# Optimization experiments

Measured on AMD Instinct MI355X. Metric: run time of the kernel, lower is better.

The kernel has to match this reference:

```python
import jax, jax.numpy as jnp
import numpy as np

NUM_EXPERT = 16
IN_FEAT = 1024
OUT_FEAT = 1024
BATCH = 8192


def setup_inputs() -> dict:
    key = jax.random.key(0)
    k_inp, k_gate, k_w = jax.random.split(key, 3)
    inp = jax.random.normal(k_inp, (BATCH, IN_FEAT), dtype=jnp.float32)
    gate = jax.random.randint(k_gate, (BATCH,), 0, NUM_EXPERT, dtype=jnp.int32)
    # nn.Linear default init: uniform(-1/sqrt(in_feat), 1/sqrt(in_feat))
    bound = 1.0 / np.sqrt(IN_FEAT)
    weight = jax.random.uniform(
        k_w, (NUM_EXPERT, OUT_FEAT, IN_FEAT), dtype=jnp.float32,
        minval=-bound, maxval=bound)
    return {"inp": inp, "gate": gate, "weight": weight}


def reference(inp, gate, weight):
    # o[t] = weight[gate[t]] @ inp[t]
    # Loop over the (small, fixed) expert axis via lax.scan; each step does a
    # dense [B, in] @ [in, out] GEMM and keeps rows routed to that expert.
    num_expert, out_feat, _ = weight.shape
    batch = inp.shape[0]

    def body(o, xs):
        i, w = xs  # w: [out_feat, in_feat]
        y = inp @ w.T  # [batch, out_feat]
        sel = (gate == i)[:, None]
        return jnp.where(sel, y, o), None

    o0 = jnp.zeros((batch, out_feat), dtype=inp.dtype)
    o, _ = jax.lax.scan(body, o0, (jnp.arange(num_expert), weight))
    return o
```

## Files before the change

### kernel.cpp

```cpp
#include <hip/hip_runtime.h>
#include <hip/hip_bf16.h>

#define NE    16
#define KDIM  1024
#define NDIM  1024
#define BATCH 8192
#define TM    128
#define TN    64
#define MAXT  96

typedef __attribute__((ext_vector_type(8))) short short8;
typedef __attribute__((ext_vector_type(4))) float floatx4;
typedef unsigned short ushort_t;

#define O_TG0  1024
#define O_TE   2048
#define O_TEND 3072
#define O_GIDX 4096
#define O_TOK  36864
#define O_PA   73728
#define WS_REQ 17113088

#define GLOAD_LDS(gp, lp) __builtin_amdgcn_global_load_lds( \
    (const __attribute__((address_space(1))) unsigned int*)(gp), \
    (__attribute__((address_space(3))) unsigned int*)(lp), 16, 0, 0)

__device__ __forceinline__ unsigned int pk2bf(float x, float y) {
    __hip_bfloat162 h = __float22bfloat162_rn(make_float2(x, y));
    unsigned int u;
    __builtin_memcpy(&u, &h, 4);
    return u;
}


__global__ __launch_bounds__(1024) void map_k(
        const int* __restrict__ gate, int* __restrict__ gidx,
        int* __restrict__ tg0, int* __restrict__ te, int* __restrict__ tend) {
    __shared__ int lc[NE];
    __shared__ int base[NE];
    const int tid = threadIdx.x;
    if (tid < NE) lc[tid] = 0;
    __syncthreads();
    int e[8], r[8];
    #pragma unroll
    for (int i = 0; i < 8; ++i) {
        int t = tid + i * 1024;
        e[i] = gate[t];
        r[i] = atomicAdd(&lc[e[i]], 1);
    }
    __syncthreads();
    if (tid == 0) {
        int o = 0, nt = 0;
        for (int j = 0; j < NE; ++j) {
            base[j] = o;
            int c = lc[j];
            for (int rr = 0; rr < c; rr += TM) {
                int r0 = (rr + TM <= c) ? rr : (c > TM ? c - TM : 0);
                tg0[nt] = o + r0; te[nt] = j; tend[nt] = o + c; ++nt;
            }
            o += c;
        }
        for (; nt < MAXT; ++nt) { tg0[nt] = 0; te[nt] = 0; tend[nt] = 0; }
    }
    __syncthreads();
    #pragma unroll
    for (int i = 0; i < 8; ++i) {
        int t = tid + i * 1024;
        gidx[t] = base[e[i]] + r[i];
    }
}

__global__ __launch_bounds__(256, 8) void gather_k(
        const float* __restrict__ inp, const int* __restrict__ gidx,
        ushort_t* __restrict__ pA, int* __restrict__ tok) {
    const int b = blockIdx.x, tid = threadIdx.x;
    const int col = (tid & 127) * 8;
    const int half = tid >> 7;
    int g[2]; float4 v0[2], v1[2];
    #pragma unroll
    for (int p = 0; p < 2; ++p) {
        int t = b * 4 + p * 2 + half;
        g[p] = gidx[t];
        v0[p] = *(const float4*)&inp[(size_t)t * KDIM + col];
        v1[p] = *(const float4*)&inp[(size_t)t * KDIM + col + 4];
    }
    #pragma unroll
    for (int p = 0; p < 2; ++p) {
        uint4 u = make_uint4(pk2bf(v0[p].x, v0[p].y), pk2bf(v0[p].z, v0[p].w),
                             pk2bf(v1[p].x, v1[p].y), pk2bf(v1[p].z, v1[p].w));
        *(uint4*)&pA[(size_t)g[p] * KDIM + col] = u;
        if (col == 0) tok[g[p]] = b * 4 + p * 2 + half;
    }
}

__global__ __launch_bounds__(256, 5) void moe_gemm5_k(
        const ushort_t* __restrict__ pA, const float* __restrict__ wgt,
        const int* __restrict__ tg0, const int* __restrict__ teArr,
        const int* __restrict__ tend, const int* __restrict__ tok,
        float* __restrict__ out) {
    const int y   = blockIdx.y;
    const int g0  = tg0[y];
    const int end = tend[y];
    if (g0 >= end) return;
    const int e    = teArr[y];
    const int out0 = blockIdx.x * TN;

    __shared__ ushort_t As[TM][64];
    __shared__ ushort_t Bs[TN][64];
    __shared__ int tok_s[TM];

    const int tid = threadIdx.x;
    if (tid < TM) tok_s[tid] = tok[g0 + tid];

    const int wave = tid >> 6, lane = tid & 63;
    const int wm = (wave >> 1) * 64;
    const int wn = (wave & 1) * 32;
    const int quad = lane >> 4, l16 = lane & 15;

    const ushort_t* Ab = pA + (size_t)g0 * KDIM;
    const float*    Bw = wgt + ((size_t)e * NDIM + out0) * KDIM;

    floatx4 acc[4][2] = {};
    const int slotw = wave * 64 + lane;

    for (int k0 = 0; k0 < KDIM; k0 += 64) {
        float4 bv[2][2];
        #pragma unroll
        for (int i = 0; i < 2; ++i) {
            int slot = i * 256 + slotw;
            int row = slot >> 3;
            int kc = (slot & 7) ^ (row & 7);
            const float* src = Bw + (size_t)row * KDIM + k0 + kc * 8;
            bv[i][0] = *(const float4*)src;
            bv[i][1] = *(const float4*)(src + 4);
        }
        #pragma unroll
        for (int i = 0; i < 4; ++i) {
            int slot = i * 256 + slotw;
            int row = slot >> 3;
            int kc = (slot & 7) ^ (row & 7);
            GLOAD_LDS(Ab + (size_t)row * KDIM + k0 + kc * 8,
                      (ushort_t*)As + (size_t)(i * 256 + wave * 64) * 8);
        }
        #pragma unroll
        for (int i = 0; i < 2; ++i) {
            int slot = i * 256 + slotw;
            uint4 u = make_uint4(pk2bf(bv[i][0].x, bv[i][0].y),
                                 pk2bf(bv[i][0].z, bv[i][0].w),
                                 pk2bf(bv[i][1].x, bv[i][1].y),
                                 pk2bf(bv[i][1].z, bv[i][1].w));
            *(uint4*)((ushort_t*)Bs + (size_t)slot * 8) = u;
        }
        __syncthreads();
        #pragma unroll
        for (int s = 0; s < 2; ++s) {
            short8 a[4], b[2];
            #pragma unroll
            for (int i = 0; i < 4; ++i) {
                int r = wm + i * 16 + l16;
                a[i] = *(const short8*)&As[r][((s * 4 + quad) ^ (r & 7)) * 8];
            }
            #pragma unroll
            for (int j = 0; j < 2; ++j) {
                int r = wn + j * 16 + l16;
                b[j] = *(const short8*)&Bs[r][((s * 4 + quad) ^ (r & 7)) * 8];
            }
            #pragma unroll
            for (int mi = 0; mi < 4; ++mi)
                #pragma unroll
                for (int nj = 0; nj < 2; ++nj)
                    acc[mi][nj] = __builtin_amdgcn_mfma_f32_16x16x32_bf16(
                        a[mi], b[nj], acc[mi][nj], 0, 0, 0);
        }
        __syncthreads();
    }

    #pragma unroll
    for (int mi = 0; mi < 4; ++mi) {
        #pragma unroll
        for (int r = 0; r < 4; ++r) {
            int lrow = wm + mi * 16 + quad * 4 + r;
            if (g0 + lrow < end) {
                int t = tok_s[lrow];
                float* orow = out + (size_t)t * NDIM + out0 + wn + l16;
                #pragma unroll
                for (int nj = 0; nj < 2; ++nj)
                    orow[nj * 16] = acc[mi][nj][r];
            }
        }
    }
}

#define LDW 20
__global__ void zero_k(int* cnt) {
    if (threadIdx.x < NE) cnt[threadIdx.x] = 0;
}

__global__ void bin_tokens_k(const int* __restrict__ gate, int* cnt, int* idx) {
    int t = blockIdx.x * blockDim.x + threadIdx.x;
    if (t < BATCH) {
        int e = gate[t];
        int p = atomicAdd(&cnt[e], 1);
        idx[e * BATCH + p] = t;
    }
}

__global__ __launch_bounds__(256) void moe_gemm_k(
        const float* __restrict__ inp, const float* __restrict__ wgt,
        const int* __restrict__ cnt, const int* __restrict__ idx,
        float* __restrict__ out) {
    const int e = blockIdx.z;
    const int n_e = cnt[e];
    const int row0 = blockIdx.y * TM;
    if (row0 >= n_e) return;
    const int out0 = blockIdx.x * 128;
    __shared__ unsigned int As[TM * LDW];
    __shared__ unsigned int Bs[TM * LDW];
    __shared__ int tok_s[TM];
    const int tid = threadIdx.x;
    if (tid < TM) {
        int g = row0 + tid;
        tok_s[tid] = (g < n_e) ? idx[e * BATCH + g] : -1;
    }
    const int wave = tid >> 6, lane = tid & 63;
    const int wm = (wave >> 1) * 64, wn = (wave & 1) * 64;
    const int quad = lane >> 4, l16 = lane & 15;
    floatx4 acc[4][4] = {};
    const int cg = (tid & 7) * 4;
    const int rbase = tid >> 3;
    const float* wbase = wgt + (size_t)e * KDIM * NDIM;
    for (int k0 = 0; k0 < KDIM; k0 += 32) {
        __syncthreads();
        #pragma unroll
        for (int p = 0; p < 4; ++p) {
            int row = p * 32 + rbase;
            int t = tok_s[row];
            float4 va = make_float4(0.f, 0.f, 0.f, 0.f);
            if (t >= 0) va = *(const float4*)&inp[(size_t)t * KDIM + k0 + cg];
            As[row * LDW + (cg >> 1)]     = pk2bf(va.x, va.y);
            As[row * LDW + (cg >> 1) + 1] = pk2bf(va.z, va.w);
            float4 vb = *(const float4*)&wbase[(size_t)(out0 + row) * KDIM + k0 + cg];
            Bs[row * LDW + (cg >> 1)]     = pk2bf(vb.x, vb.y);
            Bs[row * LDW + (cg >> 1) + 1] = pk2bf(vb.z, vb.w);
        }
        __syncthreads();
        short8 a[4], b[4];
        #pragma unroll
        for (int i = 0; i < 4; ++i)
            a[i] = *(const short8*)&As[(wm + i * 16 + l16) * LDW + quad * 4];
        #pragma unroll
        for (int i = 0; i < 4; ++i)
            b[i] = *(const short8*)&Bs[(wn + i * 16 + l16) * LDW + quad * 4];
        #pragma unroll
        for (int mi = 0; mi < 4; ++mi)
            #pragma unroll
            for (int ni = 0; ni < 4; ++ni)
                acc[mi][ni] = __builtin_amdgcn_mfma_f32_16x16x32_bf16(
                    a[mi], b[ni], acc[mi][ni], 0, 0, 0);
    }
    #pragma unroll
    for (int mi = 0; mi < 4; ++mi) {
        #pragma unroll
        for (int r = 0; r < 4; ++r) {
            int lrow = wm + mi * 16 + quad * 4 + r;
            int t = tok_s[lrow];
            if (t >= 0) {
                float* orow = out + (size_t)t * NDIM + out0 + wn + l16;
                #pragma unroll
                for (int ni = 0; ni < 4; ++ni)
                    orow[ni * 16] = acc[mi][ni][r];
            }
        }
    }
}

extern "C" void kernel_launch(void* const* d_in, const int* in_sizes, int n_in,
                              void* d_out, int out_size, void* d_ws, size_t ws_size,
                              hipStream_t stream) {
    const float* inp  = (const float*)d_in[0];
    const int*   gate = (const int*)d_in[1];
    const float* wgt  = (const float*)d_in[2];
    float*       out  = (float*)d_out;
    char* w = (char*)d_ws;

    if (ws_size >= WS_REQ) {
        int* tg0  = (int*)(w + O_TG0);
        int* te   = (int*)(w + O_TE);
        int* tend = (int*)(w + O_TEND);
        int* gidx = (int*)(w + O_GIDX);
        int* tok  = (int*)(w + O_TOK);
        ushort_t* pA = (ushort_t*)(w + O_PA);

        map_k<<<1, 1024, 0, stream>>>(gate, gidx, tg0, te, tend);
        gather_k<<<2048, 256, 0, stream>>>(inp, gidx, pA, tok);
        dim3 grid(NDIM / TN, MAXT, 1);
        moe_gemm5_k<<<grid, 256, 0, stream>>>(pA, wgt, tg0, te, tend, tok, out);
    } else {
        int* cnt = (int*)d_ws;
        int* idx = cnt + NE;
        zero_k<<<1, 64, 0, stream>>>(cnt);
        bin_tokens_k<<<BATCH / 256, 256, 0, stream>>>(gate, cnt, idx);
        dim3 grid(NDIM / 128, BATCH / TM, NE);
        moe_gemm_k<<<grid, 256, 0, stream>>>(inp, wgt, cnt, idx, out);
    }
}
```

Before: 174.4 us.

## Use ballot-based stable ranking in map kernel and swizzle GEMM block order

The token-mapping kernel drops shared-memory atomics and ranks tokens inside each wave using ballots and mbcnt, with per-chunk counts combined by a prefix scan. This gives a deterministic, ordered token placement and avoids atomic contention. The GEMM launch becomes a flat 1D grid that is remapped so groups of 8 row tiles cycle through all 16 column tiles together, aiming for better L2 reuse of activation and weight tiles. The serial 128-step scan done by 16 threads adds some latency to the single-block map kernel.

```diff
diff --git a/kernel.cpp b/kernel.cpp
--- a/kernel.cpp
+++ b/kernel.cpp
@@ -36,24 +36,50 @@
 __global__ __launch_bounds__(1024) void map_k(
         const int* __restrict__ gate, int* __restrict__ gidx,
         int* __restrict__ tg0, int* __restrict__ te, int* __restrict__ tend) {
-    __shared__ int lc[NE];
-    __shared__ int base[NE];
+    __shared__ int ccnt[128][NE];
+    __shared__ int cbase[128][NE];
+    __shared__ int ebase[NE];
+    __shared__ int etot[NE];
     const int tid = threadIdx.x;
-    if (tid < NE) lc[tid] = 0;
+    const int wv = tid >> 6, ln = tid & 63;
+
+    ((int*)ccnt)[tid] = 0;
+    ((int*)ccnt)[tid + 1024] = 0;
     __syncthreads();
-    int e[8], r[8];
+
+    int e[8], rk[8];
     #pragma unroll
     for (int i = 0; i < 8; ++i) {
-        int t = tid + i * 1024;
-        e[i] = gate[t];
-        r[i] = atomicAdd(&lc[e[i]], 1);
+        const int chunk = wv * 8 + i;
+        const int t = chunk * 64 + ln;
+        const int ei = gate[t];
+        unsigned long long m = ~0ull;
+        #pragma unroll
+        for (int b = 0; b < 4; ++b) {
+            unsigned long long bb = __ballot(((ei >> b) & 1) != 0);
+            m &= ((ei >> b) & 1) ? bb : ~bb;
+        }
+        const unsigned int lo = (unsigned int)m;
+        const unsigned int hi = (unsigned int)(m >> 32);
+        const int r = __builtin_amdgcn_mbcnt_hi(
+            hi, __builtin_amdgcn_mbcnt_lo(lo, 0));
+        if (r == 0) ccnt[chunk][ei] = __popcll(m);
+        e[i] = ei; rk[i] = r;
     }
     __syncthreads();
+
+    if (tid < NE) {
+        int s = 0;
+        for (int c = 0; c < 128; ++c) { cbase[c][tid] = s; s += ccnt[c][tid]; }
+        etot[tid] = s;
+    }
+    __syncthreads();
+
     if (tid == 0) {
         int o = 0, nt = 0;
         for (int j = 0; j < NE; ++j) {
-            base[j] = o;
-            int c = lc[j];
+            ebase[j] = o;
+            int c = etot[j];
             for (int rr = 0; rr < c; rr += TM) {
                 int r0 = (rr + TM <= c) ? rr : (c > TM ? c - TM : 0);
                 tg0[nt] = o + r0; te[nt] = j; tend[nt] = o + c; ++nt;
@@ -63,10 +89,12 @@
         for (; nt < MAXT; ++nt) { tg0[nt] = 0; te[nt] = 0; tend[nt] = 0; }
     }
     __syncthreads();
+
     #pragma unroll
     for (int i = 0; i < 8; ++i) {
-        int t = tid + i * 1024;
-        gidx[t] = base[e[i]] + r[i];
+        const int chunk = wv * 8 + i;
+        const int t = chunk * 64 + ln;
+        gidx[t] = ebase[e[i]] + cbase[chunk][e[i]] + rk[i];
     }
 }
 
@@ -98,12 +126,14 @@
         const int* __restrict__ tg0, const int* __restrict__ teArr,
         const int* __restrict__ tend, const int* __restrict__ tok,
         float* __restrict__ out) {
-    const int y   = blockIdx.y;
+    const int id  = blockIdx.x;
+    const int y   = (id & 7) + 8 * (id >> 7);
+    const int xb  = (id >> 3) & 15;
     const int g0  = tg0[y];
     const int end = tend[y];
     if (g0 >= end) return;
     const int e    = teArr[y];
-    const int out0 = blockIdx.x * TN;
+    const int out0 = xb * TN;
 
     __shared__ ushort_t As[TM][64];
     __shared__ ushort_t Bs[TN][64];
@@ -293,8 +323,7 @@
 
         map_k<<<1, 1024, 0, stream>>>(gate, gidx, tg0, te, tend);
         gather_k<<<2048, 256, 0, stream>>>(inp, gidx, pA, tok);
-        dim3 grid(NDIM / TN, MAXT, 1);
-        moe_gemm5_k<<<grid, 256, 0, stream>>>(pA, wgt, tg0, te, tend, tok, out);
+        moe_gemm5_k<<<16 * MAXT, 256, 0, stream>>>(pA, wgt, tg0, te, tend, tok, out);
     } else {
         int* cnt = (int*)d_ws;
         int* idx = cnt + NE;
```

Measured after the change: 180.3 us. 3.4% more time.
